# Performance work log

Hardware: AMD Instinct MI355X
Metric: run time of the kernel (lower is better)

## Reference

```python
import jax, jax.numpy as jnp
import numpy as np


def setup_inputs() -> dict:
    key = jax.random.key(0)
    k1, k2, k3 = jax.random.split(key, 3)
    B, N, M, D = 2, 16384, 8192, 3
    return {
        "points1": jax.random.normal(k1, (B, N, D), dtype=jnp.float32),
        "points2": jax.random.normal(k2, (B, M, D), dtype=jnp.float32),
        "weights": jax.random.normal(k3, (B, N), dtype=jnp.float32),
    }


def reference(points1, points2, weights):
    # softmax over the N points of points1
    w = jax.nn.softmax(weights, axis=1)                      # (B, N)
    sq1 = jnp.sum(points1 * points1, axis=-1)                # (B, N)
    sq2 = jnp.sum(points2 * points2, axis=-1)                # (B, M)
    cross = jnp.einsum("bnd,bmd->bnm", points1, points2)     # (B, N, M)
    dist = sq1[:, :, None] + sq2[:, None, :] - 2.0 * cross   # (B, N, M)
    min_dist1 = jnp.min(dist, axis=2)                        # (B, N)
    min_dist2 = jnp.min(dist, axis=1)                        # (B, M)
    loss_term1 = jnp.sum(w * min_dist1, axis=1)              # (B,)
    loss_term2 = jnp.mean(min_dist2, axis=1)                 # (B,)
    return jnp.mean(loss_term1 + loss_term2)
```

## Files before the change

kernel.cpp:

```cpp
#include <hip/hip_runtime.h>

#define B_ 2
#define N_ 16384
#define M_ 8192
#define CH 2

typedef float f32x4 __attribute__((ext_vector_type(4)));
typedef float f32x16 __attribute__((ext_vector_type(16)));
typedef short s16x8 __attribute__((ext_vector_type(8)));

__device__ inline float min3f(float a, float b, float c) {
    float d;
    asm("v_min3_f32 %0, %1, %2, %3" : "=v"(d) : "v"(a), "v"(b), "v"(c));
    return d;
}

__device__ inline float dpp_min_step(float v, const int ctrl) {
    int vi = __float_as_int(v);
    int s;
    switch (ctrl) {
        case 0x111: s = __builtin_amdgcn_update_dpp(vi, vi, 0x111, 0xf, 0xf, false); break;
        case 0x112: s = __builtin_amdgcn_update_dpp(vi, vi, 0x112, 0xf, 0xf, false); break;
        case 0x114: s = __builtin_amdgcn_update_dpp(vi, vi, 0x114, 0xf, 0xf, false); break;
        case 0x118: s = __builtin_amdgcn_update_dpp(vi, vi, 0x118, 0xf, 0xf, false); break;
        default:    s = __builtin_amdgcn_update_dpp(vi, vi, 0x142, 0xf, 0xf, false); break;
    }
    return fminf(v, __int_as_float(s));
}
__device__ inline float redmin32_dpp(float v) {
    v = dpp_min_step(v, 0x111);
    v = dpp_min_step(v, 0x112);
    v = dpp_min_step(v, 0x114);
    v = dpp_min_step(v, 0x118);
    v = dpp_min_step(v, 0x142);
    return v;
}

__device__ inline unsigned short f2bf(float f) {
    unsigned int u = __float_as_uint(f);
    u += 0x7FFFu + ((u >> 16) & 1u);
    return (unsigned short)(u >> 16);
}
__device__ inline float bf2f(unsigned short h) {
    return __uint_as_float(((unsigned int)h) << 16);
}
__device__ inline void split2(float v, unsigned short& hb, unsigned short& mb) {
    hb = f2bf(v);
    mb = f2bf(v - bf2f(hb));
}

#define ONE_BF ((short)0x3F80)

__device__ inline void buildA2(float x0, float x1, float x2,
                               s16x8& q0, s16x8& q1) {
    float sq = fmaf(x0, x0, fmaf(x1, x1, x2 * x2));
    unsigned short uh[3], um[3], sh, sm;
    split2(-2.f * x0, uh[0], um[0]);
    split2(-2.f * x1, uh[1], um[1]);
    split2(-2.f * x2, uh[2], um[2]);
    split2(sq, sh, sm);
    q0 = (s16x8){(short)uh[0], (short)uh[1], (short)uh[2], (short)uh[0],
                 (short)uh[1], (short)uh[2], (short)um[0], (short)um[1]};
    q1 = (s16x8){(short)um[2], (short)um[0], (short)um[1], (short)um[2],
                 (short)sh, (short)sm, ONE_BF, ONE_BF};
}
__device__ inline void buildB2(float y0, float y1, float y2,
                               s16x8& q0, s16x8& q1) {
    float sq = fmaf(y0, y0, fmaf(y1, y1, y2 * y2));
    unsigned short yh[3], ym[3], sh, sm;
    split2(y0, yh[0], ym[0]);
    split2(y1, yh[1], ym[1]);
    split2(y2, yh[2], ym[2]);
    split2(sq, sh, sm);
    q0 = (s16x8){(short)yh[0], (short)yh[1], (short)yh[2], (short)ym[0],
                 (short)ym[1], (short)ym[2], (short)yh[0], (short)yh[1]};
    q1 = (s16x8){(short)yh[2], (short)ym[0], (short)ym[1], (short)ym[2],
                 ONE_BF, ONE_BF, (short)sh, (short)sm};
}


__device__ inline float blk_reduce_max(float v, float* red) {
    #pragma unroll
    for (int off = 32; off; off >>= 1) v = fmaxf(v, __shfl_xor(v, off));
    int wid = threadIdx.x >> 6;
    int lane = threadIdx.x & 63;
    if (lane == 0) red[wid] = v;
    __syncthreads();
    if (wid == 0) {
        v = (lane < 4) ? red[lane] : -3.402823466e38f;
        #pragma unroll
        for (int off = 32; off; off >>= 1) v = fmaxf(v, __shfl_xor(v, off));
        if (lane == 0) red[0] = v;
    }
    __syncthreads();
    v = red[0];
    __syncthreads();
    return v;
}

__device__ inline float blk_reduce_sum(float v, float* red) {
    #pragma unroll
    for (int off = 32; off; off >>= 1) v += __shfl_xor(v, off);
    int wid = threadIdx.x >> 6;
    int lane = threadIdx.x & 63;
    if (lane == 0) red[wid] = v;
    __syncthreads();
    if (wid == 0) {
        v = (lane < 4) ? red[lane] : 0.0f;
        #pragma unroll
        for (int off = 32; off; off >>= 1) v += __shfl_xor(v, off);
        if (lane == 0) red[0] = v;
    }
    __syncthreads();
    v = red[0];
    __syncthreads();
    return v;
}


__global__ __launch_bounds__(256) void init_ws(const float* __restrict__ wts,
                                               const float* __restrict__ p1,
                                               const float* __restrict__ p2,
                                               unsigned int* min1, unsigned int* min2,
                                               float* __restrict__ wmax_part,
                                               unsigned int* __restrict__ ctr,
                                               s16x8* __restrict__ Afrag,
                                               s16x8* __restrict__ Bfrag,
                                               float* out) {
    int j = blockIdx.x * 256 + threadIdx.x;
    if (j < 256) ctr[j] = 0u;
    if (j == 0) out[0] = 0.0f;
    if (j < B_ * N_) {
        min1[j] = 0x7F7FFFFFu;
        float v = wts[j];
        #pragma unroll
        for (int off = 32; off; off >>= 1) v = fmaxf(v, __shfl_xor(v, off));
        if ((j & 63) == 0) wmax_part[j >> 6] = v;

        int b = j >> 14, n = j & (N_ - 1);
        const float* px = p1 + (size_t)j * 3;
        s16x8 q0, q1;
        buildA2(px[0], px[1], px[2], q0, q1);
        Afrag[((size_t)b * 2 + 0) * N_ + n] = q0;
        Afrag[((size_t)b * 2 + 1) * N_ + n] = q1;
    } else {
        int k = j - B_ * N_;
        min2[k] = 0x7F7FFFFFu;
        int b = k >> 13, m = k & (M_ - 1);
        const float* py = p2 + (size_t)k * 3;
        s16x8 q0, q1;
        buildB2(py[0], py[1], py[2], q0, q1);
        Bfrag[((size_t)b * 2 + 0) * M_ + m] = q0;
        Bfrag[((size_t)b * 2 + 1) * M_ + m] = q1;
    }
}

__global__ __launch_bounds__(256) void chamfer_mfma(
        const s16x8* __restrict__ Afrag, const s16x8* __restrict__ Bfrag,
        unsigned int* __restrict__ min1, unsigned int* __restrict__ min2) {
    __shared__ s16x8 Bsh[4][256];
    __shared__ float scr[4][16][2][32];

    const int bid = blockIdx.x;
    const int b   = bid >> 10;
    const int rr  = bid & 1023;
    const int ob  = rr >> 4;
    const int bin = rr & 15;
    const int nb    = ob * 256;
    const int mbase = bin * (CH * 256);

    const int t = threadIdx.x;
    const int w = t >> 6, l = t & 63;
    const int lc = l & 31, lh = l >> 5;

    const s16x8* Ab = Afrag + (size_t)(b * 2) * N_;
    const s16x8* Bb = Bfrag + (size_t)(b * 2) * M_;
    unsigned int* m1g = min1 + (size_t)b * N_;
    unsigned int* m2g = min2 + (size_t)b * M_;

    s16x8 b0 = Bb[0 * M_ + mbase + t];
    s16x8 b1 = Bb[1 * M_ + mbase + t];
    s16x8 b2 = Bb[0 * M_ + mbase + 256 + t];
    s16x8 b3 = Bb[1 * M_ + mbase + 256 + t];
    {
        s16x8* As = (s16x8*)scr;
        As[0 * 256 + t] = Ab[0 * N_ + nb + t];
        As[1 * 256 + t] = Ab[1 * N_ + nb + t];
    }
    __syncthreads();
    s16x8 Af0, Af1;
    {
        const s16x8* As = (const s16x8*)scr;
        Af0 = As[lh * 256 + w * 64 + lc];
        Af1 = As[lh * 256 + w * 64 + 32 + lc];
    }
    __syncthreads();
    Bsh[0][t] = b0;
    Bsh[1][t] = b1;
    Bsh[2][t] = b2;
    Bsh[3][t] = b3;
    __syncthreads();

    f32x16 mn1a, mn1b;
    #pragma unroll
    for (int i = 0; i < 16; i++) { mn1a[i] = 3.402823466e38f; mn1b[i] = 3.402823466e38f; }
    f32x16 zacc;
    #pragma unroll
    for (int i = 0; i < 16; i++) zacc[i] = 0.f;

    #pragma unroll 2
    for (int it = 0; it < CH * 8; it++) {
        const int c = it >> 3, mt = it & 7;
        s16x8 Bf = Bsh[c * 2 + lh][mt * 32 + lc];
        f32x16 aA = __builtin_amdgcn_mfma_f32_32x32x16_bf16(Af0, Bf, zacc, 0, 0, 0);
        f32x16 aB = __builtin_amdgcn_mfma_f32_32x32x16_bf16(Af1, Bf, zacc, 0, 0, 0);
        #pragma unroll
        for (int i = 0; i < 16; i++) {
            mn1a[i] = fminf(mn1a[i], aA[i]);
            mn1b[i] = fminf(mn1b[i], aB[i]);
        }
        float f0 = min3f(aA[0], aA[1], aA[2]);
        float f1 = min3f(aA[3], aA[4], aA[5]);
        float f2 = min3f(aA[6], aA[7], aA[8]);
        float f3 = min3f(aA[9], aA[10], aA[11]);
        float f4 = min3f(aA[12], aA[13], aA[14]);
        float f5 = min3f(aA[15], aB[0], aB[1]);
        float f6 = min3f(aB[2], aB[3], aB[4]);
        float f7 = min3f(aB[5], aB[6], aB[7]);
        float f8 = min3f(aB[8], aB[9], aB[10]);
        float f9 = min3f(aB[11], aB[12], aB[13]);
        float g0 = min3f(f0, f1, f2);
        float g1 = min3f(f3, f4, f5);
        float g2 = min3f(f6, f7, f8);
        float g3 = min3f(f9, aB[14], aB[15]);
        float m2 = fminf(fminf(g0, g1), fminf(g2, g3));
        scr[w][it][lh][lc] = m2;
    }

    __syncthreads();

    #pragma unroll
    for (int rep = 0; rep < 2; rep++) {
        int cid = rep * 256 + t;
        int c = cid >> 8, rem = cid & 255;
        int slot = c * 8 + (rem >> 5), cc = rem & 31;
        float v = fminf(
            fminf(fminf(scr[0][slot][0][cc], scr[0][slot][1][cc]),
                  fminf(scr[1][slot][0][cc], scr[1][slot][1][cc])),
            fminf(fminf(scr[2][slot][0][cc], scr[2][slot][1][cc]),
                  fminf(scr[3][slot][0][cc], scr[3][slot][1][cc])));
        atomicMin(&m2g[mbase + cid], __float_as_uint(v));
    }

    #pragma unroll
    for (int i = 0; i < 16; i++) {
        float v = redmin32_dpp(mn1a[i]);
        float u = redmin32_dpp(mn1b[i]);
        if (lc == 31) {
            int row = nb + w * 64 + (i & 3) + 8 * (i >> 2) + 4 * lh;
            atomicMin(&m1g[row], __float_as_uint(v));
            atomicMin(&m1g[row + 32], __float_as_uint(u));
        }
    }
}

__global__ __launch_bounds__(256) void finalize_wide(
        const float* __restrict__ wts,
        const unsigned int* __restrict__ min1,
        const unsigned int* __restrict__ min2,
        const float* __restrict__ wmax_part,
        unsigned int* __restrict__ ctr,
        float* __restrict__ out) {
    __shared__ float red[4];
    __shared__ unsigned tk_sh;
    unsigned int* cntF = ctr + 160;
    float* acc = (float*)(ctr + 168);

    const int blk = blockIdx.x;
    const int t = threadIdx.x;

    if (blk < 32) {
        int b = blk >> 4, sl = blk & 15;
        float lm = wmax_part[b * 256 + t];
        float gmax = blk_reduce_max(lm, red);
        int base = b * N_ + sl * 1024;
        float se = 0.f, swm = 0.f;
        #pragma unroll
        for (int i = 0; i < 4; i++) {
            int idx = base + i * 256 + t;
            float e = expf(wts[idx] - gmax);
            se += e;
            swm += e * __uint_as_float(min1[idx]);
        }
        float tse = blk_reduce_sum(se, red);
        float tswm = blk_reduce_sum(swm, red);
        if (t == 0) {
            atomicAdd(&acc[b * 3 + 0], tse);
            atomicAdd(&acc[b * 3 + 1], tswm);
        }
    } else {
        int k = blk - 32;
        int b = k >> 3, sl = k & 7;
        int base = b * M_ + sl * 1024;
        float s = 0.f;
        #pragma unroll
        for (int i = 0; i < 4; i++)
            s += __uint_as_float(min2[base + i * 256 + t]);
        float ts = blk_reduce_sum(s, red);
        if (t == 0) atomicAdd(&acc[b * 3 + 2], ts);
    }

    asm volatile("s_waitcnt vmcnt(0)" ::: "memory");
    __syncthreads();
    if (t == 0) tk_sh = atomicAdd(cntF, 1u);
    __syncthreads();
    if (tk_sh == 47u && t == 0) {
        float s0 = atomicAdd(&acc[0], 0.0f);
        float s1 = atomicAdd(&acc[1], 0.0f);
        float s2 = atomicAdd(&acc[2], 0.0f);
        float s3 = atomicAdd(&acc[3], 0.0f);
        float s4 = atomicAdd(&acc[4], 0.0f);
        float s5 = atomicAdd(&acc[5], 0.0f);
        out[0] = ((s1 / s0 + s2 * (1.0f / (float)M_)) +
                  (s4 / s3 + s5 * (1.0f / (float)M_))) * (1.0f / (float)B_);
    }
}


extern "C" void kernel_launch(void* const* d_in, const int* in_sizes, int n_in,
                              void* d_out, int out_size, void* d_ws, size_t ws_size,
                              hipStream_t stream) {
    const float* p1  = (const float*)d_in[0];
    const float* p2  = (const float*)d_in[1];
    const float* wts = (const float*)d_in[2];
    float* out = (float*)d_out;

    unsigned int* min1 = (unsigned int*)d_ws;
    unsigned int* min2 = min1 + B_ * N_;
    float* wmax_part = (float*)(min2 + B_ * M_);
    unsigned int* ctr = (unsigned int*)(wmax_part + 512);
    char* frag_base = (char*)d_ws + 196608 + 4096;
    s16x8* Afrag = (s16x8*)frag_base;
    s16x8* Bfrag = Afrag + B_ * 2 * N_;

    init_ws<<<dim3((B_ * N_ + B_ * M_) / 256), dim3(256), 0, stream>>>(
        wts, p1, p2, min1, min2, wmax_part, ctr, Afrag, Bfrag, out);
    chamfer_mfma<<<dim3(B_ * (N_ / 256) * (M_ / (CH * 256))), dim3(256), 0, stream>>>(
        Afrag, Bfrag, min1, min2);
    finalize_wide<<<dim3(48), dim3(256), 0, stream>>>(
        wts, min1, min2, wmax_part, ctr, out);
}
```

Before: 40.86 us.

## Widen per-block M range fourfold and restage B tiles in quarters

Each block now covers 2048 columns of points2 instead of 512, so the grid shrinks fourfold. All B fragments are preloaded into registers up front and staged into shared memory one quarter at a time, with a column-min combine after each quarter. Because each block covers more columns, it issues fewer row-min atomics and reloads its A fragments less often. In exchange, far fewer blocks run, which lowers occupancy and parallelism on the GPU, and the sixteen preloaded fragments add register pressure.

```diff
diff --git a/kernel.cpp b/kernel.cpp
--- a/kernel.cpp
+++ b/kernel.cpp
@@ -3,7 +3,7 @@
 #define B_ 2
 #define N_ 16384
 #define M_ 8192
-#define CH 2
+#define CH 8
 
 typedef float f32x4 __attribute__((ext_vector_type(4)));
 typedef float f32x16 __attribute__((ext_vector_type(16)));
@@ -162,10 +162,10 @@
     __shared__ float scr[4][16][2][32];
 
     const int bid = blockIdx.x;
-    const int b   = bid >> 10;
-    const int rr  = bid & 1023;
-    const int ob  = rr >> 4;
-    const int bin = rr & 15;
+    const int b   = bid >> 8;
+    const int rr  = bid & 255;
+    const int ob  = rr >> 2;
+    const int bin = rr & 3;
     const int nb    = ob * 256;
     const int mbase = bin * (CH * 256);
 
@@ -178,10 +178,22 @@
     unsigned int* m1g = min1 + (size_t)b * N_;
     unsigned int* m2g = min2 + (size_t)b * M_;
 
-    s16x8 b0 = Bb[0 * M_ + mbase + t];
-    s16x8 b1 = Bb[1 * M_ + mbase + t];
-    s16x8 b2 = Bb[0 * M_ + mbase + 256 + t];
-    s16x8 b3 = Bb[1 * M_ + mbase + 256 + t];
+    s16x8 b0  = Bb[0 * M_ + mbase + t];
+    s16x8 b1  = Bb[1 * M_ + mbase + t];
+    s16x8 b2  = Bb[0 * M_ + mbase + 256 + t];
+    s16x8 b3  = Bb[1 * M_ + mbase + 256 + t];
+    s16x8 b4  = Bb[0 * M_ + mbase + 512 + t];
+    s16x8 b5  = Bb[1 * M_ + mbase + 512 + t];
+    s16x8 b6  = Bb[0 * M_ + mbase + 768 + t];
+    s16x8 b7  = Bb[1 * M_ + mbase + 768 + t];
+    s16x8 b8  = Bb[0 * M_ + mbase + 1024 + t];
+    s16x8 b9  = Bb[1 * M_ + mbase + 1024 + t];
+    s16x8 b10 = Bb[0 * M_ + mbase + 1280 + t];
+    s16x8 b11 = Bb[1 * M_ + mbase + 1280 + t];
+    s16x8 b12 = Bb[0 * M_ + mbase + 1536 + t];
+    s16x8 b13 = Bb[1 * M_ + mbase + 1536 + t];
+    s16x8 b14 = Bb[0 * M_ + mbase + 1792 + t];
+    s16x8 b15 = Bb[1 * M_ + mbase + 1792 + t];
     {
         s16x8* As = (s16x8*)scr;
         As[0 * 256 + t] = Ab[0 * N_ + nb + t];
@@ -208,49 +220,76 @@
     #pragma unroll
     for (int i = 0; i < 16; i++) zacc[i] = 0.f;
 
-    #pragma unroll 2
-    for (int it = 0; it < CH * 8; it++) {
-        const int c = it >> 3, mt = it & 7;
-        s16x8 Bf = Bsh[c * 2 + lh][mt * 32 + lc];
-        f32x16 aA = __builtin_amdgcn_mfma_f32_32x32x16_bf16(Af0, Bf, zacc, 0, 0, 0);
-        f32x16 aB = __builtin_amdgcn_mfma_f32_32x32x16_bf16(Af1, Bf, zacc, 0, 0, 0);
-        #pragma unroll
-        for (int i = 0; i < 16; i++) {
-            mn1a[i] = fminf(mn1a[i], aA[i]);
-            mn1b[i] = fminf(mn1b[i], aB[i]);
-        }
-        float f0 = min3f(aA[0], aA[1], aA[2]);
-        float f1 = min3f(aA[3], aA[4], aA[5]);
-        float f2 = min3f(aA[6], aA[7], aA[8]);
-        float f3 = min3f(aA[9], aA[10], aA[11]);
-        float f4 = min3f(aA[12], aA[13], aA[14]);
-        float f5 = min3f(aA[15], aB[0], aB[1]);
-        float f6 = min3f(aB[2], aB[3], aB[4]);
-        float f7 = min3f(aB[5], aB[6], aB[7]);
-        float f8 = min3f(aB[8], aB[9], aB[10]);
-        float f9 = min3f(aB[11], aB[12], aB[13]);
-        float g0 = min3f(f0, f1, f2);
-        float g1 = min3f(f3, f4, f5);
-        float g2 = min3f(f6, f7, f8);
-        float g3 = min3f(f9, aB[14], aB[15]);
-        float m2 = fminf(fminf(g0, g1), fminf(g2, g3));
-        scr[w][it][lh][lc] = m2;
-    }
-
-    __syncthreads();
-
-    #pragma unroll
-    for (int rep = 0; rep < 2; rep++) {
-        int cid = rep * 256 + t;
-        int c = cid >> 8, rem = cid & 255;
-        int slot = c * 8 + (rem >> 5), cc = rem & 31;
-        float v = fminf(
-            fminf(fminf(scr[0][slot][0][cc], scr[0][slot][1][cc]),
-                  fminf(scr[1][slot][0][cc], scr[1][slot][1][cc])),
-            fminf(fminf(scr[2][slot][0][cc], scr[2][slot][1][cc]),
-                  fminf(scr[3][slot][0][cc], scr[3][slot][1][cc])));
-        atomicMin(&m2g[mbase + cid], __float_as_uint(v));
-    }
+    #define QUARTER_BODY                                                        \
+        _Pragma("unroll 2")                                                     \
+        for (int it = 0; it < 16; it++) {                                       \
+            const int c = it >> 3, mt = it & 7;                                 \
+            s16x8 Bf = Bsh[c * 2 + lh][mt * 32 + lc];                           \
+            f32x16 aA = __builtin_amdgcn_mfma_f32_32x32x16_bf16(Af0, Bf, zacc, 0, 0, 0); \
+            f32x16 aB = __builtin_amdgcn_mfma_f32_32x32x16_bf16(Af1, Bf, zacc, 0, 0, 0); \
+            _Pragma("unroll")                                                   \
+            for (int i = 0; i < 16; i++) {                                      \
+                mn1a[i] = fminf(mn1a[i], aA[i]);                                \
+                mn1b[i] = fminf(mn1b[i], aB[i]);                                \
+            }                                                                   \
+            float f0 = min3f(aA[0], aA[1], aA[2]);                              \
+            float f1 = min3f(aA[3], aA[4], aA[5]);                              \
+            float f2 = min3f(aA[6], aA[7], aA[8]);                              \
+            float f3 = min3f(aA[9], aA[10], aA[11]);                            \
+            float f4 = min3f(aA[12], aA[13], aA[14]);                           \
+            float f5 = min3f(aA[15], aB[0], aB[1]);                             \
+            float f6 = min3f(aB[2], aB[3], aB[4]);                              \
+            float f7 = min3f(aB[5], aB[6], aB[7]);                              \
+            float f8 = min3f(aB[8], aB[9], aB[10]);                             \
+            float f9 = min3f(aB[11], aB[12], aB[13]);                           \
+            float g0 = min3f(f0, f1, f2);                                       \
+            float g1 = min3f(f3, f4, f5);                                       \
+            float g2 = min3f(f6, f7, f8);                                       \
+            float g3 = min3f(f9, aB[14], aB[15]);                               \
+            float m2 = fminf(fminf(g0, g1), fminf(g2, g3));                     \
+            scr[w][it][lh][lc] = m2;                                            \
+        }
+
+    #define QUARTER_COMBINE(q)                                                  \
+        _Pragma("unroll")                                                       \
+        for (int rep = 0; rep < 2; rep++) {                                     \
+            int cid = rep * 256 + t;                                            \
+            int c = cid >> 8, rem = cid & 255;                                  \
+            int slot = c * 8 + (rem >> 5), cc = rem & 31;                       \
+            float v = fminf(                                                    \
+                fminf(fminf(scr[0][slot][0][cc], scr[0][slot][1][cc]),          \
+                      fminf(scr[1][slot][0][cc], scr[1][slot][1][cc])),         \
+                fminf(fminf(scr[2][slot][0][cc], scr[2][slot][1][cc]),          \
+                      fminf(scr[3][slot][0][cc], scr[3][slot][1][cc])));        \
+            atomicMin(&m2g[mbase + (q) * 512 + cid], __float_as_uint(v));       \
+        }
+
+    #define RESTAGE(x0, x1, x2, x3)                                             \
+        Bsh[0][t] = x0; Bsh[1][t] = x1; Bsh[2][t] = x2; Bsh[3][t] = x3;         \
+        __syncthreads();
+
+    QUARTER_BODY
+    __syncthreads();
+    QUARTER_COMBINE(0)
+    RESTAGE(b4, b5, b6, b7)
+
+    QUARTER_BODY
+    __syncthreads();
+    QUARTER_COMBINE(1)
+    RESTAGE(b8, b9, b10, b11)
+
+    QUARTER_BODY
+    __syncthreads();
+    QUARTER_COMBINE(2)
+    RESTAGE(b12, b13, b14, b15)
+
+    QUARTER_BODY
+    __syncthreads();
+    QUARTER_COMBINE(3)
+
+    #undef QUARTER_BODY
+    #undef QUARTER_COMBINE
+    #undef RESTAGE
 
     #pragma unroll
     for (int i = 0; i < 16; i++) {
```

After: 38.43 us. 6.0% less time.
